# Kernel optimization log

Hardware: AMD Instinct MI355X
Metric: run time of the kernel (lower is better)

Reference implementation:

```python
import jax, jax.numpy as jnp
import numpy as np

LATENT = 128
LN_EPS = 1e-3  # keras LayerNormalization default epsilon


def _mlp(x, W0, b0, W1, b1, W2, b2, gamma, beta):
    # two relu hidden layers + linear output + layer norm (MeshGraphNets style)
    h = jax.nn.relu(x @ W0 + b0)
    h = jax.nn.relu(h @ W1 + b1)
    h = h @ W2 + b2
    mu = jnp.mean(h, axis=-1, keepdims=True)
    var = jnp.var(h, axis=-1, keepdims=True)
    return (h - mu) * jax.lax.rsqrt(var + LN_EPS) * gamma + beta


def setup_inputs() -> dict:
    key = jax.random.key(0)
    ks = jax.random.split(key, 12)
    N, D, E = 10000, 128, 320000
    cat = 3 * D  # sender + receiver + edge features concatenated
    s = lambda fan: 1.0 / np.sqrt(fan)
    return {
        "sender_features": jax.random.normal(ks[0], (N, D), jnp.float32),
        "receiver_features": jax.random.normal(ks[1], (N, D), jnp.float32),
        "edge_features": jax.random.normal(ks[2], (E, D), jnp.float32),
        "senders": jax.random.randint(ks[3], (E,), 0, N, jnp.int32),
        "receivers": jax.random.randint(ks[4], (E,), 0, N, jnp.int32),
        "W0": jax.random.normal(ks[5], (cat, LATENT), jnp.float32) * s(cat),
        "b0": jnp.zeros((LATENT,), jnp.float32),
        "W1": jax.random.normal(ks[6], (LATENT, LATENT), jnp.float32) * s(LATENT),
        "b1": jnp.zeros((LATENT,), jnp.float32),
        "W2": jax.random.normal(ks[7], (LATENT, LATENT), jnp.float32) * s(LATENT),
        "b2": jnp.zeros((LATENT,), jnp.float32),
        "gamma": jnp.ones((LATENT,), jnp.float32),
        "beta": jnp.zeros((LATENT,), jnp.float32),
    }


def reference(sender_features, receiver_features, edge_features, senders,
              receivers, W0, b0, W1, b1, W2, b2, gamma, beta):
    g_send = jnp.take(sender_features, senders, axis=0)      # [E, D]
    g_recv = jnp.take(receiver_features, receivers, axis=0)  # [E, D]
    feats = jnp.concatenate([g_send, g_recv, edge_features], axis=-1)  # [E, 3D]
    return _mlp(feats, W0, b0, W1, b1, W2, b2, gamma, beta)  # [E, LATENT]
```

## Files before the change

### kernel.cpp

```cpp
#include <hip/hip_runtime.h>
#include <stdint.h>


typedef __attribute__((ext_vector_type(8)))  short    s16x8;
typedef __attribute__((ext_vector_type(8)))  _Float16 f16x8;
typedef __attribute__((ext_vector_type(16))) float    f32x16;
typedef __attribute__((ext_vector_type(4)))  float    f32x4;

#define FENCE asm volatile("" ::: "memory")
#define VMWAIT(N) asm volatile("s_waitcnt vmcnt(" #N ")" ::: "memory")
#define BARRIER do { __builtin_amdgcn_s_barrier(); asm volatile("" ::: "memory"); } while (0)

__device__ __forceinline__ f32x16 mfma16(f16x8 a, f16x8 b, f32x16 c) {
  return __builtin_amdgcn_mfma_f32_32x32x16_f16(a, b, c, 0, 0, 0);
}

__global__ void prep_weights(const float* __restrict__ W0,
                             const float* __restrict__ W1,
                             const float* __restrict__ W2,
                             short* __restrict__ ws) {
  int tid = blockIdx.x * 256 + threadIdx.x;
  const float* W;
  int rel, imgbase, perm;
  if (tid < 6144)      { W = W0; rel = tid;        imgbase = 0;     perm = 0; }
  else if (tid < 8192) { W = W1; rel = tid - 6144; imgbase = 49152; perm = 1; }
  else                 { W = W2; rel = tid - 8192; imgbase = 65536; perm = 1; }
  int n     = rel & 127;
  int chunk = rel >> 7;
  int slab  = chunk >> 3;
  int kc    = chunk & 7;
  s16x8 o;
#pragma unroll
  for (int j = 0; j < 8; ++j) {
    int kslot = slab * 64 + kc * 8 + j;
    int ktrue = perm ? ((kslot & ~12) | ((kslot & 4) << 1) | ((kslot & 8) >> 1))
                     : kslot;
    float v = W[(size_t)ktrue * 128 + n];
    o[j] = __builtin_bit_cast(short, (_Float16)v);
  }
  *(s16x8*)(ws + imgbase + slab * 8192 + n * 64 + ((kc ^ (n & 7)) << 3)) = o;
}

__device__ __forceinline__ void stage(const short* __restrict__ ws, int s,
                                      int slot, char* lds, int tid) {
  char* buf = lds + slot * 16384;
  const char* g = (const char*)ws + s * 16384;
#pragma unroll
  for (int i = 0; i < 2; ++i) {
    char* lp = buf + (i * 512 + (tid & ~63)) * 16;
    const char* gp = g + (i * 512 + tid) * 16;
    __builtin_amdgcn_global_load_lds(
        (__attribute__((address_space(1))) const void*)gp,
        (__attribute__((address_space(3))) void*)lp, 16, 0, 0);
  }
}

__device__ __forceinline__ void kstep(const char* buf, int q, int lg1,
                                      int e31, f16x8 xf, f32x16* acc) {
  const int kc = q * 2 + lg1;
  const int slot = (kc ^ (e31 & 7)) << 4;
#pragma unroll
  for (int nt = 0; nt < 4; ++nt) {
    int n = nt * 32 + e31;
    s16x8 wf = *(const s16x8*)(buf + n * 128 + slot);
    acc[nt] = mfma16(__builtin_bit_cast(f16x8, wf), xf, acc[nt]);
  }
}

__device__ __forceinline__ void transition(const float* __restrict__ b,
                                           int lg1, f32x16* acc, f16x8* fr) {
#pragma unroll
  for (int ks = 0; ks < 8; ++ks) {
    const int nt = ks >> 1;
#pragma unroll
    for (int jq = 0; jq < 2; ++jq) {
      int nb = nt * 32 + 16 * (ks & 1) + 8 * jq + 4 * lg1;
      f32x4 bv = *(const f32x4*)(b + nb);
#pragma unroll
      for (int r = 0; r < 4; ++r) {
        float h = acc[nt][8 * (ks & 1) + jq * 4 + r] + bv[r];
        fr[ks][jq * 4 + r] = (_Float16)fmaxf(h, 0.0f);
      }
    }
  }
}

__device__ __forceinline__ void zero_acc(f32x16* acc) {
#pragma unroll
  for (int nt = 0; nt < 4; ++nt)
#pragma unroll
    for (int i = 0; i < 16; ++i) acc[nt][i] = 0.0f;
}

__global__ __launch_bounds__(512, 4) void edge_mlp(
    const float* __restrict__ sf, const float* __restrict__ rf,
    const float* __restrict__ ef, const int* __restrict__ snd,
    const int* __restrict__ rcv, const short* __restrict__ wt,
    const float* __restrict__ b0, const float* __restrict__ b1,
    const float* __restrict__ b2, const float* __restrict__ gamma,
    const float* __restrict__ beta, float* __restrict__ out) {
  __shared__ __align__(16) char lds[52224];
  const int tid  = threadIdx.x;
  const int w    = tid >> 6;
  const int lane = tid & 63;
  const int e31  = lane & 31;
  const int lg1  = lane >> 5;
  const int eb   = blockIdx.x * 256 + w * 32;
  const int e    = eb + e31;

  if (w < 3) {
    const float* s0 = (w == 0) ? b0 : (w == 1) ? b2 : beta;
    const float* s1 = (w == 0) ? b1 : (w == 1) ? gamma : beta;
    const float* src = ((lane < 32) ? s0 : s1) + (lane & 31) * 4;
    char* dst = lds + 49152 + w * 1024;
    __builtin_amdgcn_global_load_lds(
        (__attribute__((address_space(1))) const void*)src,
        (__attribute__((address_space(3))) void*)dst, 16, 0, 0);
  }
  FENCE;
  const int sidx = snd[e];
  const int ridx = rcv[e];
  FENCE;
  stage(wt, 0, 0, lds, tid);
  FENCE;
  stage(wt, 1, 1, lds, tid);
  FENCE;

  const float* xbase0 = sf + (size_t)sidx * 128 + lg1 * 8;
  const float* xbase1 = rf + (size_t)ridx * 128 + lg1 * 8;
  const float* xbase2 = ef + (size_t)e    * 128 + lg1 * 8;
#define XPTR(t) ((t) < 8 ? xbase0 + (t) * 16 \
                : (t) < 16 ? xbase1 + ((t) - 8) * 16 \
                : xbase2 + ((t) - 16) * 16)
#define XISSUE(t) do { const float* p_ = XPTR(t); \
    xa[(t) % 5] = *(const f32x4*)p_; xb[(t) % 5] = *(const f32x4*)(p_ + 4); } while (0)
#define KSTEP0(t, buf) do { \
    f16x8 xf_; f32x4 A_ = xa[(t) % 5], B_ = xb[(t) % 5]; \
    xf_[0]=(_Float16)A_[0]; xf_[1]=(_Float16)A_[1]; xf_[2]=(_Float16)A_[2]; xf_[3]=(_Float16)A_[3]; \
    xf_[4]=(_Float16)B_[0]; xf_[5]=(_Float16)B_[1]; xf_[6]=(_Float16)B_[2]; xf_[7]=(_Float16)B_[3]; \
    kstep((buf), (t) & 3, lg1, e31, xf_, acc); } while (0)

  f32x16 acc[4];
  zero_acc(acc);
  f32x4 xa[5], xb[5];
  XISSUE(0); XISSUE(1); XISSUE(2); XISSUE(3); XISSUE(4);
  FENCE;
  VMWAIT(12); BARRIER;

  f16x8 fr[8];

  { const char* buf = lds;
    stage(wt, 2, 2, lds, tid);
    KSTEP0(0, buf); XISSUE(5);
    KSTEP0(1, buf); XISSUE(6);
    KSTEP0(2, buf); XISSUE(7);
    KSTEP0(3, buf); XISSUE(8);
    VMWAIT(20); BARRIER; }
  { const char* buf = lds + 16384;
    stage(wt, 3, 0, lds, tid);
    KSTEP0(4, buf); XISSUE(9);
    KSTEP0(5, buf); XISSUE(10);
    KSTEP0(6, buf); XISSUE(11);
    KSTEP0(7, buf); XISSUE(12);
    VMWAIT(18); BARRIER; }
  { const char* buf = lds + 32768;
    stage(wt, 4, 1, lds, tid);
    KSTEP0(8, buf); XISSUE(13);
    KSTEP0(9, buf); XISSUE(14);
    KSTEP0(10, buf); XISSUE(15);
    KSTEP0(11, buf); XISSUE(16);
    VMWAIT(18); BARRIER; }
  { const char* buf = lds;
    stage(wt, 5, 2, lds, tid);
    KSTEP0(12, buf); XISSUE(17);
    KSTEP0(13, buf); XISSUE(18);
    KSTEP0(14, buf); XISSUE(19);
    KSTEP0(15, buf); XISSUE(20);
    VMWAIT(18); BARRIER; }
  { const char* buf = lds + 16384;
    stage(wt, 6, 0, lds, tid);
    KSTEP0(16, buf); XISSUE(21);
    KSTEP0(17, buf); XISSUE(22);
    KSTEP0(18, buf); XISSUE(23);
    KSTEP0(19, buf);
    VMWAIT(16); BARRIER; }
  { const char* buf = lds + 32768;
    stage(wt, 7, 1, lds, tid);
    KSTEP0(20, buf);
    KSTEP0(21, buf);
    KSTEP0(22, buf);
    KSTEP0(23, buf);
    transition((const float*)(lds + 49152), lg1, acc, fr);
    zero_acc(acc);
    VMWAIT(8); BARRIER; }

  { const char* buf = lds;
    stage(wt, 8, 2, lds, tid);
    kstep(buf, 0, lg1, e31, fr[0], acc);
    kstep(buf, 1, lg1, e31, fr[1], acc);
    kstep(buf, 2, lg1, e31, fr[2], acc);
    kstep(buf, 3, lg1, e31, fr[3], acc);
    VMWAIT(2); BARRIER; }
  { const char* buf = lds + 16384;
    stage(wt, 9, 0, lds, tid);
    kstep(buf, 0, lg1, e31, fr[4], acc);
    kstep(buf, 1, lg1, e31, fr[5], acc);
    kstep(buf, 2, lg1, e31, fr[6], acc);
    kstep(buf, 3, lg1, e31, fr[7], acc);
    transition((const float*)(lds + 49152 + 512), lg1, acc, fr);
    zero_acc(acc);
    VMWAIT(2); BARRIER; }

  { const char* buf = lds + 32768;
    kstep(buf, 0, lg1, e31, fr[0], acc);
    kstep(buf, 1, lg1, e31, fr[1], acc);
    kstep(buf, 2, lg1, e31, fr[2], acc);
    kstep(buf, 3, lg1, e31, fr[3], acc);
    VMWAIT(0); BARRIER; }
  { const char* buf = lds;
    kstep(buf, 0, lg1, e31, fr[4], acc);
    kstep(buf, 1, lg1, e31, fr[5], acc);
    kstep(buf, 2, lg1, e31, fr[6], acc);
    kstep(buf, 3, lg1, e31, fr[7], acc);
  }
  BARRIER;

  const float* pb2 = (const float*)(lds + 49152 + 1024);
  const float* pg  = (const float*)(lds + 49152 + 1536);
  const float* pbt = (const float*)(lds + 49152 + 2048);
  float sum = 0.f, sq = 0.f;
#pragma unroll
  for (int nt = 0; nt < 4; ++nt)
#pragma unroll
    for (int qq = 0; qq < 4; ++qq) {
      f32x4 bv = *(const f32x4*)(pb2 + nt * 32 + qq * 8 + 4 * lg1);
#pragma unroll
      for (int r = 0; r < 4; ++r) {
        float v = acc[nt][qq * 4 + r] + bv[r];
        acc[nt][qq * 4 + r] = v;
        sum += v; sq += v * v;
      }
    }
  sum += __shfl_xor(sum, 32, 64);
  sq  += __shfl_xor(sq, 32, 64);
  const float mu = sum * (1.0f / 128.0f);
  const float rs = rsqrtf(sq * (1.0f / 128.0f) - mu * mu + 1e-3f);

  float* T = (float*)lds + w * 1056;
  const int l4 = lane >> 2, ch = lane & 3;
#pragma unroll
  for (int p = 0; p < 4; ++p) {
#pragma unroll
    for (int qq = 0; qq < 4; ++qq) {
      const int n0 = p * 32 + qq * 8 + 4 * lg1;
      f32x4 g4 = *(const f32x4*)(pg + n0);
      f32x4 t4 = *(const f32x4*)(pbt + n0);
#pragma unroll
      for (int r = 0; r < 4; ++r)
        T[e31 * 33 + qq * 8 + 4 * lg1 + r] =
            (acc[p][qq * 4 + r] - mu) * rs * g4[r] + t4[r];
    }
#pragma unroll
    for (int bb = 0; bb < 2; ++bb) {
      const int el = bb * 16 + l4;
      float* orow = out + (size_t)(eb + el) * 128 + p * 32 + ch * 4;
#pragma unroll
      for (int j = 0; j < 2; ++j) {
        f32x4 ov;
#pragma unroll
        for (int k = 0; k < 4; ++k) ov[k] = T[el * 33 + j * 16 + ch * 4 + k];
        *(f32x4*)(orow + j * 16) = ov;
      }
    }
  }
#undef XPTR
#undef XISSUE
#undef KSTEP0
}

extern "C" void kernel_launch(void* const* d_in, const int* in_sizes, int n_in,
                              void* d_out, int out_size, void* d_ws, size_t ws_size,
                              hipStream_t stream) {
  const float* sf    = (const float*)d_in[0];
  const float* rf    = (const float*)d_in[1];
  const float* ef    = (const float*)d_in[2];
  const int*   snd   = (const int*)d_in[3];
  const int*   rcv   = (const int*)d_in[4];
  const float* W0    = (const float*)d_in[5];
  const float* b0    = (const float*)d_in[6];
  const float* W1    = (const float*)d_in[7];
  const float* b1    = (const float*)d_in[8];
  const float* W2    = (const float*)d_in[9];
  const float* b2    = (const float*)d_in[10];
  const float* gamma = (const float*)d_in[11];
  const float* beta  = (const float*)d_in[12];
  short* wt = (short*)d_ws;

  prep_weights<<<40, 256, 0, stream>>>(W0, W1, W2, wt);
  edge_mlp<<<1250, 512, 0, stream>>>(sf, rf, ef, snd, rcv, wt,
                                     b0, b1, b2, gamma, beta, (float*)d_out);
}
```

Baseline: 441.3 us.

## Shrink edge-MLP blocks to 256 threads and simplify pipeline synchronization

Workgroups shrink from 512 to 256 threads (128 edges each) and the grid doubles. The hand-tuned vmcnt waits and asm fences are replaced by plain __syncthreads, and biases, gamma and beta are read from global memory instead of being staged in LDS. W0 rows are reordered so the contiguous edge-feature slice is consumed first, and the LDS swizzle gains an extra XOR term meant to reduce bank conflicts. The goal is more resident blocks per CU and simpler scheduling, but the coarser barriers may drain more of the load pipelining, and the weight slabs are now loaded per 128 edges instead of per 256.

Result: faster. 425.3 us (-3.6%).

```diff
diff --git a/kernel.cpp b/kernel.cpp
--- a/kernel.cpp
+++ b/kernel.cpp
@@ -6,10 +6,6 @@
 typedef __attribute__((ext_vector_type(8)))  _Float16 f16x8;
 typedef __attribute__((ext_vector_type(16))) float    f32x16;
 typedef __attribute__((ext_vector_type(4)))  float    f32x4;
-
-#define FENCE asm volatile("" ::: "memory")
-#define VMWAIT(N) asm volatile("s_waitcnt vmcnt(" #N ")" ::: "memory")
-#define BARRIER do { __builtin_amdgcn_s_barrier(); asm volatile("" ::: "memory"); } while (0)
 
 __device__ __forceinline__ f32x16 mfma16(f16x8 a, f16x8 b, f32x16 c) {
   return __builtin_amdgcn_mfma_f32_32x32x16_f16(a, b, c, 0, 0, 0);
@@ -21,10 +17,10 @@
                              short* __restrict__ ws) {
   int tid = blockIdx.x * 256 + threadIdx.x;
   const float* W;
-  int rel, imgbase, perm;
-  if (tid < 6144)      { W = W0; rel = tid;        imgbase = 0;     perm = 0; }
-  else if (tid < 8192) { W = W1; rel = tid - 6144; imgbase = 49152; perm = 1; }
-  else                 { W = W2; rel = tid - 8192; imgbase = 65536; perm = 1; }
+  int rel, imgbase, kind;
+  if (tid < 6144)      { W = W0; rel = tid;        imgbase = 0;     kind = 0; }
+  else if (tid < 8192) { W = W1; rel = tid - 6144; imgbase = 49152; kind = 1; }
+  else                 { W = W2; rel = tid - 8192; imgbase = 65536; kind = 1; }
   int n     = rel & 127;
   int chunk = rel >> 7;
   int slab  = chunk >> 3;
@@ -33,12 +29,16 @@
 #pragma unroll
   for (int j = 0; j < 8; ++j) {
     int kslot = slab * 64 + kc * 8 + j;
-    int ktrue = perm ? ((kslot & ~12) | ((kslot & 4) << 1) | ((kslot & 8) >> 1))
-                     : kslot;
+    int ktrue;
+    if (kind == 0)
+      ktrue = (kslot < 128) ? kslot + 256 : kslot - 128;
+    else
+      ktrue = (kslot & ~12) | ((kslot & 4) << 1) | ((kslot & 8) >> 1);
     float v = W[(size_t)ktrue * 128 + n];
     o[j] = __builtin_bit_cast(short, (_Float16)v);
   }
-  *(s16x8*)(ws + imgbase + slab * 8192 + n * 64 + ((kc ^ (n & 7)) << 3)) = o;
+  int slot = kc ^ (n & 7) ^ ((n >> 3) & 3);
+  *(s16x8*)(ws + imgbase + slab * 8192 + n * 64 + (slot << 3)) = o;
 }
 
 __device__ __forceinline__ void stage(const short* __restrict__ ws, int s,
@@ -46,9 +46,9 @@
   char* buf = lds + slot * 16384;
   const char* g = (const char*)ws + s * 16384;
 #pragma unroll
-  for (int i = 0; i < 2; ++i) {
-    char* lp = buf + (i * 512 + (tid & ~63)) * 16;
-    const char* gp = g + (i * 512 + tid) * 16;
+  for (int i = 0; i < 4; ++i) {
+    char* lp = buf + (i * 256 + (tid & ~63)) * 16;
+    const char* gp = g + (i * 256 + tid) * 16;
     __builtin_amdgcn_global_load_lds(
         (__attribute__((address_space(1))) const void*)gp,
         (__attribute__((address_space(3))) void*)lp, 16, 0, 0);
@@ -58,11 +58,11 @@
 __device__ __forceinline__ void kstep(const char* buf, int q, int lg1,
                                       int e31, f16x8 xf, f32x16* acc) {
   const int kc = q * 2 + lg1;
-  const int slot = (kc ^ (e31 & 7)) << 4;
 #pragma unroll
   for (int nt = 0; nt < 4; ++nt) {
     int n = nt * 32 + e31;
-    s16x8 wf = *(const s16x8*)(buf + n * 128 + slot);
+    int slot = kc ^ (e31 & 7) ^ ((e31 >> 3) & 3);
+    s16x8 wf = *(const s16x8*)(buf + n * 128 + (slot << 4));
     acc[nt] = mfma16(__builtin_bit_cast(f16x8, wf), xf, acc[nt]);
   }
 }
@@ -92,148 +92,129 @@
     for (int i = 0; i < 16; ++i) acc[nt][i] = 0.0f;
 }
 
-__global__ __launch_bounds__(512, 4) void edge_mlp(
+__global__ __launch_bounds__(256, 3) void edge_mlp(
     const float* __restrict__ sf, const float* __restrict__ rf,
     const float* __restrict__ ef, const int* __restrict__ snd,
     const int* __restrict__ rcv, const short* __restrict__ wt,
     const float* __restrict__ b0, const float* __restrict__ b1,
     const float* __restrict__ b2, const float* __restrict__ gamma,
     const float* __restrict__ beta, float* __restrict__ out) {
-  __shared__ __align__(16) char lds[52224];
+  __shared__ __align__(16) char lds[49152];
   const int tid  = threadIdx.x;
   const int w    = tid >> 6;
   const int lane = tid & 63;
   const int e31  = lane & 31;
   const int lg1  = lane >> 5;
-  const int eb   = blockIdx.x * 256 + w * 32;
+  const int eb   = blockIdx.x * 128 + w * 32;
   const int e    = eb + e31;
 
-  if (w < 3) {
-    const float* s0 = (w == 0) ? b0 : (w == 1) ? b2 : beta;
-    const float* s1 = (w == 0) ? b1 : (w == 1) ? gamma : beta;
-    const float* src = ((lane < 32) ? s0 : s1) + (lane & 31) * 4;
-    char* dst = lds + 49152 + w * 1024;
-    __builtin_amdgcn_global_load_lds(
-        (__attribute__((address_space(1))) const void*)src,
-        (__attribute__((address_space(3))) void*)dst, 16, 0, 0);
-  }
-  FENCE;
   const int sidx = snd[e];
   const int ridx = rcv[e];
-  FENCE;
   stage(wt, 0, 0, lds, tid);
-  FENCE;
   stage(wt, 1, 1, lds, tid);
-  FENCE;
-
-  const float* xbase0 = sf + (size_t)sidx * 128 + lg1 * 8;
-  const float* xbase1 = rf + (size_t)ridx * 128 + lg1 * 8;
-  const float* xbase2 = ef + (size_t)e    * 128 + lg1 * 8;
+
+  const float* xbase0 = ef + (size_t)e    * 128 + lg1 * 8;
+  const float* xbase1 = sf + (size_t)sidx * 128 + lg1 * 8;
+  const float* xbase2 = rf + (size_t)ridx * 128 + lg1 * 8;
 #define XPTR(t) ((t) < 8 ? xbase0 + (t) * 16 \
                 : (t) < 16 ? xbase1 + ((t) - 8) * 16 \
                 : xbase2 + ((t) - 16) * 16)
 #define XISSUE(t) do { const float* p_ = XPTR(t); \
-    xa[(t) % 5] = *(const f32x4*)p_; xb[(t) % 5] = *(const f32x4*)(p_ + 4); } while (0)
+    xa[(t) % 4] = *(const f32x4*)p_; xb[(t) % 4] = *(const f32x4*)(p_ + 4); } while (0)
 #define KSTEP0(t, buf) do { \
-    f16x8 xf_; f32x4 A_ = xa[(t) % 5], B_ = xb[(t) % 5]; \
+    f16x8 xf_; f32x4 A_ = xa[(t) % 4], B_ = xb[(t) % 4]; \
     xf_[0]=(_Float16)A_[0]; xf_[1]=(_Float16)A_[1]; xf_[2]=(_Float16)A_[2]; xf_[3]=(_Float16)A_[3]; \
     xf_[4]=(_Float16)B_[0]; xf_[5]=(_Float16)B_[1]; xf_[6]=(_Float16)B_[2]; xf_[7]=(_Float16)B_[3]; \
     kstep((buf), (t) & 3, lg1, e31, xf_, acc); } while (0)
 
   f32x16 acc[4];
   zero_acc(acc);
-  f32x4 xa[5], xb[5];
-  XISSUE(0); XISSUE(1); XISSUE(2); XISSUE(3); XISSUE(4);
-  FENCE;
-  VMWAIT(12); BARRIER;
-
+  f32x4 xa[4], xb[4];
+  XISSUE(0); XISSUE(1); XISSUE(2); XISSUE(3);
   f16x8 fr[8];
 
+  __syncthreads();
   { const char* buf = lds;
     stage(wt, 2, 2, lds, tid);
-    KSTEP0(0, buf); XISSUE(5);
-    KSTEP0(1, buf); XISSUE(6);
-    KSTEP0(2, buf); XISSUE(7);
-    KSTEP0(3, buf); XISSUE(8);
-    VMWAIT(20); BARRIER; }
+    KSTEP0(0, buf);  XISSUE(4);
+    KSTEP0(1, buf);  XISSUE(5);
+    KSTEP0(2, buf);  XISSUE(6);
+    KSTEP0(3, buf);  XISSUE(7); }
+  __syncthreads();
   { const char* buf = lds + 16384;
     stage(wt, 3, 0, lds, tid);
-    KSTEP0(4, buf); XISSUE(9);
-    KSTEP0(5, buf); XISSUE(10);
-    KSTEP0(6, buf); XISSUE(11);
-    KSTEP0(7, buf); XISSUE(12);
-    VMWAIT(18); BARRIER; }
+    KSTEP0(4, buf);  XISSUE(8);
+    KSTEP0(5, buf);  XISSUE(9);
+    KSTEP0(6, buf);  XISSUE(10);
+    KSTEP0(7, buf);  XISSUE(11); }
+  __syncthreads();
   { const char* buf = lds + 32768;
     stage(wt, 4, 1, lds, tid);
-    KSTEP0(8, buf); XISSUE(13);
-    KSTEP0(9, buf); XISSUE(14);
-    KSTEP0(10, buf); XISSUE(15);
-    KSTEP0(11, buf); XISSUE(16);
-    VMWAIT(18); BARRIER; }
+    KSTEP0(8, buf);  XISSUE(12);
+    KSTEP0(9, buf);  XISSUE(13);
+    KSTEP0(10, buf); XISSUE(14);
+    KSTEP0(11, buf); XISSUE(15); }
+  __syncthreads();
   { const char* buf = lds;
     stage(wt, 5, 2, lds, tid);
-    KSTEP0(12, buf); XISSUE(17);
-    KSTEP0(13, buf); XISSUE(18);
-    KSTEP0(14, buf); XISSUE(19);
-    KSTEP0(15, buf); XISSUE(20);
-    VMWAIT(18); BARRIER; }
+    KSTEP0(12, buf); XISSUE(16);
+    KSTEP0(13, buf); XISSUE(17);
+    KSTEP0(14, buf); XISSUE(18);
+    KSTEP0(15, buf); XISSUE(19); }
+  __syncthreads();
   { const char* buf = lds + 16384;
     stage(wt, 6, 0, lds, tid);
-    KSTEP0(16, buf); XISSUE(21);
-    KSTEP0(17, buf); XISSUE(22);
-    KSTEP0(18, buf); XISSUE(23);
-    KSTEP0(19, buf);
-    VMWAIT(16); BARRIER; }
+    KSTEP0(16, buf); XISSUE(20);
+    KSTEP0(17, buf); XISSUE(21);
+    KSTEP0(18, buf); XISSUE(22);
+    KSTEP0(19, buf); XISSUE(23); }
+  __syncthreads();
   { const char* buf = lds + 32768;
     stage(wt, 7, 1, lds, tid);
     KSTEP0(20, buf);
     KSTEP0(21, buf);
     KSTEP0(22, buf);
     KSTEP0(23, buf);
-    transition((const float*)(lds + 49152), lg1, acc, fr);
-    zero_acc(acc);
-    VMWAIT(8); BARRIER; }
-
+    transition(b0, lg1, acc, fr);
+    zero_acc(acc); }
+
+  __syncthreads();
   { const char* buf = lds;
     stage(wt, 8, 2, lds, tid);
     kstep(buf, 0, lg1, e31, fr[0], acc);
     kstep(buf, 1, lg1, e31, fr[1], acc);
     kstep(buf, 2, lg1, e31, fr[2], acc);
-    kstep(buf, 3, lg1, e31, fr[3], acc);
-    VMWAIT(2); BARRIER; }
+    kstep(buf, 3, lg1, e31, fr[3], acc); }
+  __syncthreads();
   { const char* buf = lds + 16384;
     stage(wt, 9, 0, lds, tid);
     kstep(buf, 0, lg1, e31, fr[4], acc);
     kstep(buf, 1, lg1, e31, fr[5], acc);
     kstep(buf, 2, lg1, e31, fr[6], acc);
     kstep(buf, 3, lg1, e31, fr[7], acc);
-    transition((const float*)(lds + 49152 + 512), lg1, acc, fr);
-    zero_acc(acc);
-    VMWAIT(2); BARRIER; }
-
+    transition(b1, lg1, acc, fr);
+    zero_acc(acc); }
+
+  __syncthreads();
   { const char* buf = lds + 32768;
     kstep(buf, 0, lg1, e31, fr[0], acc);
     kstep(buf, 1, lg1, e31, fr[1], acc);
     kstep(buf, 2, lg1, e31, fr[2], acc);
-    kstep(buf, 3, lg1, e31, fr[3], acc);
-    VMWAIT(0); BARRIER; }
+    kstep(buf, 3, lg1, e31, fr[3], acc); }
+  __syncthreads();
   { const char* buf = lds;
     kstep(buf, 0, lg1, e31, fr[4], acc);
     kstep(buf, 1, lg1, e31, fr[5], acc);
     kstep(buf, 2, lg1, e31, fr[6], acc);
-    kstep(buf, 3, lg1, e31, fr[7], acc);
-  }
-  BARRIER;
-
-  const float* pb2 = (const float*)(lds + 49152 + 1024);
-  const float* pg  = (const float*)(lds + 49152 + 1536);
-  const float* pbt = (const float*)(lds + 49152 + 2048);
+    kstep(buf, 3, lg1, e31, fr[7], acc); }
+  __syncthreads();
+
   float sum = 0.f, sq = 0.f;
 #pragma unroll
   for (int nt = 0; nt < 4; ++nt)
 #pragma unroll
     for (int qq = 0; qq < 4; ++qq) {
-      f32x4 bv = *(const f32x4*)(pb2 + nt * 32 + qq * 8 + 4 * lg1);
+      f32x4 bv = *(const f32x4*)(b2 + nt * 32 + qq * 8 + 4 * lg1);
 #pragma unroll
       for (int r = 0; r < 4; ++r) {
         float v = acc[nt][qq * 4 + r] + bv[r];
@@ -246,15 +227,15 @@
   const float mu = sum * (1.0f / 128.0f);
   const float rs = rsqrtf(sq * (1.0f / 128.0f) - mu * mu + 1e-3f);
 
-  float* T = (float*)lds + w * 1056;
+  float* T = (float*)(lds + 16384) + w * 1056;
   const int l4 = lane >> 2, ch = lane & 3;
 #pragma unroll
   for (int p = 0; p < 4; ++p) {
 #pragma unroll
     for (int qq = 0; qq < 4; ++qq) {
       const int n0 = p * 32 + qq * 8 + 4 * lg1;
-      f32x4 g4 = *(const f32x4*)(pg + n0);
-      f32x4 t4 = *(const f32x4*)(pbt + n0);
+      f32x4 g4 = *(const f32x4*)(gamma + n0);
+      f32x4 t4 = *(const f32x4*)(beta + n0);
 #pragma unroll
       for (int r = 0; r < 4; ++r)
         T[e31 * 33 + qq * 8 + 4 * lg1 + r] =
@@ -297,6 +278,6 @@
   short* wt = (short*)d_ws;
 
   prep_weights<<<40, 256, 0, stream>>>(W0, W1, W2, wt);
-  edge_mlp<<<1250, 512, 0, stream>>>(sf, rf, ef, snd, rcv, wt,
+  edge_mlp<<<2500, 256, 0, stream>>>(sf, rf, ef, snd, rcv, wt,
                                      b0, b1, b2, gamma, beta, (float*)d_out);
 }
```
